# Performance work log

Hardware: AMD Instinct MI355X
Metric: run time of the kernel (lower is better)

The kernel has to match this reference:

```python
import jax, jax.numpy as jnp
import numpy as np

COMMITMENT_COST = 0.25


def setup_inputs() -> dict:
    key = jax.random.key(0)
    k1, k2 = jax.random.split(key)
    B, C, H, W = 64, 64, 32, 32
    K = 1024
    inputs = jax.random.normal(k1, (B, C, H, W), dtype=jnp.float32)
    # matches torch init: uniform_(-1/K, 1/K)
    weight = jax.random.uniform(k2, (K, C), dtype=jnp.float32,
                                minval=-1.0 / K, maxval=1.0 / K)
    return {"inputs": inputs, "weight": weight}


def reference(inputs, weight):
    B, C, H, W = inputs.shape
    # (B H W) C
    flat = inputs.transpose(0, 2, 3, 1).reshape(-1, C)
    distances = (jnp.sum(flat * flat, axis=1, keepdims=True)
                 + jnp.sum(weight * weight, axis=1)
                 - 2.0 * (flat @ weight.T))  # [BHW, K]
    encoding_indices = jnp.argmin(distances, axis=1)  # [BHW]
    # one-hot matmul in the original == direct gather
    quantized = jnp.take(weight, encoding_indices, axis=0)  # [BHW, C]
    quantized = quantized.reshape(B, H, W, C).transpose(0, 3, 1, 2)  # B C H W
    e_latent_loss = jnp.mean(
        (jax.lax.stop_gradient(quantized) - inputs) ** 2, axis=(1, 2, 3))
    q_latent_loss = jnp.mean(
        (quantized - jax.lax.stop_gradient(inputs)) ** 2, axis=(1, 2, 3))
    loss = q_latent_loss + COMMITMENT_COST * e_latent_loss  # [B]
    # straight-through estimator
    quantized_st = inputs + jax.lax.stop_gradient(quantized - inputs)
    indices = encoding_indices.reshape(B, H, W)
    return quantized_st, indices, loss
```

## Files before the change

kernel.cpp:

```cpp
#include <hip/hip_runtime.h>
#include <hip/hip_bf16.h>


#define VQ_C    64
#define VQ_K    1024
#define VQ_HW   1024
#define VQ_B    64
#define VQ_ROWS (VQ_B * VQ_HW)
#define BLOCK   256
#define NBLOCKS (VQ_ROWS / BLOCK)
#define NSEG    4
#define SK      (VQ_K / NSEG)

__global__ __launch_bounds__(BLOCK, 4) void vq_partial_kernel(
    const float* __restrict__ inp,
    const float* __restrict__ w,
    float* __restrict__ dist_ws,
    int*   __restrict__ idx_ws)
{
    __shared__ float se2[SK];

    const int tid = threadIdx.x;
    const int seg = blockIdx.y;
    const int k0  = seg * SK;

    {
        const float* wr = w + (size_t)(k0 + tid) * VQ_C;
        float s0 = 0.f, s1 = 0.f, s2 = 0.f, s3 = 0.f;
        #pragma unroll
        for (int c = 0; c < VQ_C; c += 4) {
            s0 = fmaf(wr[c + 0], wr[c + 0], s0);
            s1 = fmaf(wr[c + 1], wr[c + 1], s1);
            s2 = fmaf(wr[c + 2], wr[c + 2], s2);
            s3 = fmaf(wr[c + 3], wr[c + 3], s3);
        }
        se2[tid] = (s0 + s1) + (s2 + s3);
    }
    __syncthreads();

    const int r  = blockIdx.x * BLOCK + tid;
    const int b  = r >> 10;
    const int hw = r & (VQ_HW - 1);

    const float* xin = inp + (size_t)b * (VQ_C * VQ_HW) + hw;
    float x[VQ_C];
    #pragma unroll
    for (int c = 0; c < VQ_C; ++c) x[c] = xin[(size_t)c * VQ_HW];

    #pragma unroll
    for (int c = 0; c < VQ_C; ++c) asm volatile("" : "+v"(x[c]));

    float sx0 = 0.f, sx1 = 0.f, sx2 = 0.f, sx3 = 0.f;
    #pragma unroll
    for (int c = 0; c < VQ_C; c += 4) {
        sx0 = fmaf(x[c + 0], x[c + 0], sx0);
        sx1 = fmaf(x[c + 1], x[c + 1], sx1);
        sx2 = fmaf(x[c + 2], x[c + 2], sx2);
        sx3 = fmaf(x[c + 3], x[c + 3], sx3);
    }
    const float sx = (sx0 + sx1) + (sx2 + sx3);

    float best  = 3.402823466e38f;
    int   bestk = k0;
    const float* wseg = w + (size_t)k0 * VQ_C;
    #pragma unroll 2
    for (int k = 0; k < SK; ++k) {
        const float* wr = wseg + (size_t)k * VQ_C;
        float d0 = 0.f, d1 = 0.f, d2 = 0.f, d3 = 0.f;
        #pragma unroll
        for (int c = 0; c < VQ_C; c += 4) {
            d0 = fmaf(wr[c + 0], x[c + 0], d0);
            d1 = fmaf(wr[c + 1], x[c + 1], d1);
            d2 = fmaf(wr[c + 2], x[c + 2], d2);
            d3 = fmaf(wr[c + 3], x[c + 3], d3);
        }
        const float dot = (d0 + d1) + (d2 + d3);
        const float d = (sx + se2[k]) - 2.f * dot;
        if (d < best) { best = d; bestk = k0 + k; }
    }

    dist_ws[(size_t)seg * VQ_ROWS + r] = best;
    idx_ws [(size_t)seg * VQ_ROWS + r] = bestk;
}

__global__ __launch_bounds__(BLOCK) void vq_finalize_kernel(
    const float* __restrict__ inp,
    const float* __restrict__ w,
    const float* __restrict__ dist_ws,
    const int*   __restrict__ idx_ws,
    float* __restrict__ out_q,
    float* __restrict__ out_idx,
    float* __restrict__ partials)
{
    __shared__ float red[BLOCK];
    const int tid = threadIdx.x;
    const int r   = blockIdx.x * BLOCK + tid;
    const int b   = r >> 10;
    const int hw  = r & (VQ_HW - 1);

    float best  = dist_ws[r];
    int   bestk = idx_ws[r];
    #pragma unroll
    for (int s = 1; s < NSEG; ++s) {
        const float d  = dist_ws[(size_t)s * VQ_ROWS + r];
        const int   kk = idx_ws [(size_t)s * VQ_ROWS + r];
        if (d < best) { best = d; bestk = kk; }
    }

    const float* xin  = inp + (size_t)b * (VQ_C * VQ_HW) + hw;
    const float* q    = w + (size_t)bestk * VQ_C;
    float*       outr = out_q + (size_t)b * (VQ_C * VQ_HW) + hw;

    float sd0 = 0.f, sd1 = 0.f, sd2 = 0.f, sd3 = 0.f;
    #pragma unroll
    for (int c = 0; c < VQ_C; c += 4) {
        float x0 = xin[(size_t)(c + 0) * VQ_HW];
        float x1 = xin[(size_t)(c + 1) * VQ_HW];
        float x2 = xin[(size_t)(c + 2) * VQ_HW];
        float x3 = xin[(size_t)(c + 3) * VQ_HW];
        float q0 = q[c + 0], q1 = q[c + 1], q2 = q[c + 2], q3 = q[c + 3];
        outr[(size_t)(c + 0) * VQ_HW] = x0 + (q0 - x0);
        outr[(size_t)(c + 1) * VQ_HW] = x1 + (q1 - x1);
        outr[(size_t)(c + 2) * VQ_HW] = x2 + (q2 - x2);
        outr[(size_t)(c + 3) * VQ_HW] = x3 + (q3 - x3);
        float e0 = q0 - x0, e1 = q1 - x1, e2 = q2 - x2, e3 = q3 - x3;
        sd0 = fmaf(e0, e0, sd0);
        sd1 = fmaf(e1, e1, sd1);
        sd2 = fmaf(e2, e2, sd2);
        sd3 = fmaf(e3, e3, sd3);
    }
    out_idx[r] = (float)bestk;

    red[tid] = (sd0 + sd1) + (sd2 + sd3);
    __syncthreads();
    #pragma unroll
    for (int s = BLOCK / 2; s > 0; s >>= 1) {
        if (tid < s) red[tid] += red[tid + s];
        __syncthreads();
    }
    if (tid == 0) partials[blockIdx.x] = red[0];
}

__global__ __launch_bounds__(64) void vq_loss_kernel(
    const float* __restrict__ partials,
    float* __restrict__ loss)
{
    const int b = threadIdx.x;
    const float s = (partials[4 * b + 0] + partials[4 * b + 1])
                  + (partials[4 * b + 2] + partials[4 * b + 3]);
    const float L = s * (1.0f / 65536.0f);
    loss[b] = L + 0.25f * L;
}

__global__ __launch_bounds__(BLOCK) void vq_main_kernel(
    const float* __restrict__ inp,
    const float* __restrict__ w,
    float* __restrict__ out_q,
    float* __restrict__ out_idx,
    float* __restrict__ partials)
{
    __shared__ float se2[VQ_K];
    __shared__ float red[BLOCK];
    const int tid = threadIdx.x;

    for (int k = tid; k < VQ_K; k += BLOCK) {
        const float* wr = w + k * VQ_C;
        float s0 = 0.f, s1 = 0.f, s2 = 0.f, s3 = 0.f;
        #pragma unroll
        for (int c = 0; c < VQ_C; c += 4) {
            s0 = fmaf(wr[c + 0], wr[c + 0], s0);
            s1 = fmaf(wr[c + 1], wr[c + 1], s1);
            s2 = fmaf(wr[c + 2], wr[c + 2], s2);
            s3 = fmaf(wr[c + 3], wr[c + 3], s3);
        }
        se2[k] = (s0 + s1) + (s2 + s3);
    }
    __syncthreads();

    const int r  = blockIdx.x * BLOCK + tid;
    const int b  = r >> 10;
    const int hw = r & (VQ_HW - 1);

    const float* xin = inp + (size_t)b * (VQ_C * VQ_HW) + hw;
    float x[VQ_C];
    #pragma unroll
    for (int c = 0; c < VQ_C; ++c) x[c] = xin[(size_t)c * VQ_HW];
    #pragma unroll
    for (int c = 0; c < VQ_C; ++c) asm volatile("" : "+v"(x[c]));

    float sx0 = 0.f, sx1 = 0.f, sx2 = 0.f, sx3 = 0.f;
    #pragma unroll
    for (int c = 0; c < VQ_C; c += 4) {
        sx0 = fmaf(x[c + 0], x[c + 0], sx0);
        sx1 = fmaf(x[c + 1], x[c + 1], sx1);
        sx2 = fmaf(x[c + 2], x[c + 2], sx2);
        sx3 = fmaf(x[c + 3], x[c + 3], sx3);
    }
    const float sx = (sx0 + sx1) + (sx2 + sx3);

    float best = 3.402823466e38f;
    int bestk = 0;
    for (int k = 0; k < VQ_K; ++k) {
        const float* wr = w + (size_t)k * VQ_C;
        float d0 = 0.f, d1 = 0.f, d2 = 0.f, d3 = 0.f;
        #pragma unroll
        for (int c = 0; c < VQ_C; c += 4) {
            d0 = fmaf(wr[c + 0], x[c + 0], d0);
            d1 = fmaf(wr[c + 1], x[c + 1], d1);
            d2 = fmaf(wr[c + 2], x[c + 2], d2);
            d3 = fmaf(wr[c + 3], x[c + 3], d3);
        }
        const float dot = (d0 + d1) + (d2 + d3);
        const float d = (sx + se2[k]) - 2.f * dot;
        if (d < best) { best = d; bestk = k; }
    }

    const float* q = w + (size_t)bestk * VQ_C;
    float* outr = out_q + (size_t)b * (VQ_C * VQ_HW) + hw;
    float sd0 = 0.f, sd1 = 0.f, sd2 = 0.f, sd3 = 0.f;
    #pragma unroll
    for (int c = 0; c < VQ_C; c += 4) {
        float q0 = q[c + 0], q1 = q[c + 1], q2 = q[c + 2], q3 = q[c + 3];
        float x0 = x[c + 0], x1 = x[c + 1], x2 = x[c + 2], x3 = x[c + 3];
        outr[(size_t)(c + 0) * VQ_HW] = x0 + (q0 - x0);
        outr[(size_t)(c + 1) * VQ_HW] = x1 + (q1 - x1);
        outr[(size_t)(c + 2) * VQ_HW] = x2 + (q2 - x2);
        outr[(size_t)(c + 3) * VQ_HW] = x3 + (q3 - x3);
        float e0 = q0 - x0, e1 = q1 - x1, e2 = q2 - x2, e3 = q3 - x3;
        sd0 = fmaf(e0, e0, sd0);
        sd1 = fmaf(e1, e1, sd1);
        sd2 = fmaf(e2, e2, sd2);
        sd3 = fmaf(e3, e3, sd3);
    }
    out_idx[r] = (float)bestk;

    red[tid] = (sd0 + sd1) + (sd2 + sd3);
    __syncthreads();
    #pragma unroll
    for (int s = BLOCK / 2; s > 0; s >>= 1) {
        if (tid < s) red[tid] += red[tid + s];
        __syncthreads();
    }
    if (tid == 0) partials[blockIdx.x] = red[0];
}

extern "C" void kernel_launch(void* const* d_in, const int* in_sizes, int n_in,
                              void* d_out, int out_size, void* d_ws, size_t ws_size,
                              hipStream_t stream) {
    const float* inp = (const float*)d_in[0];
    const float* w   = (const float*)d_in[1];

    float* out_q    = (float*)d_out;
    float* out_idx  = (float*)d_out + 4194304;
    float* out_loss = (float*)d_out + 4194304 + 65536;

    const size_t dist_bytes = (size_t)NSEG * VQ_ROWS * sizeof(float);
    const size_t idx_bytes  = (size_t)NSEG * VQ_ROWS * sizeof(int);
    const size_t part_bytes = (size_t)NBLOCKS * sizeof(float);
    const size_t need = dist_bytes + idx_bytes + part_bytes;

    if (ws_size >= need) {
        float* dist_ws  = (float*)d_ws;
        int*   idx_ws   = (int*)((char*)d_ws + dist_bytes);
        float* partials = (float*)((char*)d_ws + dist_bytes + idx_bytes);

        vq_partial_kernel<<<dim3(NBLOCKS, NSEG), BLOCK, 0, stream>>>(inp, w, dist_ws, idx_ws);
        vq_finalize_kernel<<<NBLOCKS, BLOCK, 0, stream>>>(inp, w, dist_ws, idx_ws,
                                                          out_q, out_idx, partials);
        vq_loss_kernel<<<1, 64, 0, stream>>>(partials, out_loss);
    } else {
        float* partials = (float*)d_ws;
        vq_main_kernel<<<NBLOCKS, BLOCK, 0, stream>>>(inp, w, out_q, out_idx, partials);
        vq_loss_kernel<<<1, 64, 0, stream>>>(partials, out_loss);
    }
}
```

Baseline: 126.5 us.

## Load codebook rows via scalar s_load into SGPRs and precompute norms in separate kernel

The per-segment codebook norm computation moves into a separate small kernel that writes norms to workspace, removing the shared-memory prologue and barrier from the partial kernel. The inner distance loop now fetches each codebook row (64 floats) and its norm with inline-asm s_load_dwordx16 into scalar registers, so the FMAs take a wave-uniform SGPR operand instead of issuing vector loads. This adds an extra kernel launch and serializes each iteration on an lgkmcnt(0) wait with no unrolling, which may expose scalar-load latency.

```diff
diff --git a/kernel.cpp b/kernel.cpp
--- a/kernel.cpp
+++ b/kernel.cpp
@@ -12,70 +12,94 @@
 #define NSEG    4
 #define SK      (VQ_K / NSEG)
 
-__global__ __launch_bounds__(BLOCK, 4) void vq_partial_kernel(
+typedef float f32x16 __attribute__((ext_vector_type(16)));
+
+#define XC(c) ((c) < 16 ? x0[(c) & 15] : (c) < 32 ? x1[(c) & 15] \
+               : (c) < 48 ? x2[(c) & 15] : x3[(c) & 15])
+#define WC(c) ((c) < 16 ? w0[(c) & 15] : (c) < 32 ? w1[(c) & 15] \
+               : (c) < 48 ? w2[(c) & 15] : w3[(c) & 15])
+
+__global__ __launch_bounds__(BLOCK) void vq_se2_kernel(
+    const float* __restrict__ w, float* __restrict__ se2g) {
+    const int k = blockIdx.x * BLOCK + threadIdx.x;
+    const float* wr = w + (size_t)k * VQ_C;
+    float s0 = 0.f, s1 = 0.f, s2 = 0.f, s3 = 0.f;
+    #pragma unroll
+    for (int c = 0; c < VQ_C; c += 4) {
+        s0 = fmaf(wr[c + 0], wr[c + 0], s0);
+        s1 = fmaf(wr[c + 1], wr[c + 1], s1);
+        s2 = fmaf(wr[c + 2], wr[c + 2], s2);
+        s3 = fmaf(wr[c + 3], wr[c + 3], s3);
+    }
+    se2g[k] = (s0 + s1) + (s2 + s3);
+}
+
+__global__ void
+__attribute__((amdgpu_flat_work_group_size(BLOCK, BLOCK), amdgpu_waves_per_eu(4, 4)))
+vq_partial(
     const float* __restrict__ inp,
     const float* __restrict__ w,
+    const float* __restrict__ se2g,
     float* __restrict__ dist_ws,
     int*   __restrict__ idx_ws)
 {
-    __shared__ float se2[SK];
-
     const int tid = threadIdx.x;
     const int seg = blockIdx.y;
     const int k0  = seg * SK;
 
-    {
-        const float* wr = w + (size_t)(k0 + tid) * VQ_C;
-        float s0 = 0.f, s1 = 0.f, s2 = 0.f, s3 = 0.f;
-        #pragma unroll
-        for (int c = 0; c < VQ_C; c += 4) {
-            s0 = fmaf(wr[c + 0], wr[c + 0], s0);
-            s1 = fmaf(wr[c + 1], wr[c + 1], s1);
-            s2 = fmaf(wr[c + 2], wr[c + 2], s2);
-            s3 = fmaf(wr[c + 3], wr[c + 3], s3);
-        }
-        se2[tid] = (s0 + s1) + (s2 + s3);
-    }
-    __syncthreads();
-
     const int r  = blockIdx.x * BLOCK + tid;
     const int b  = r >> 10;
     const int hw = r & (VQ_HW - 1);
 
     const float* xin = inp + (size_t)b * (VQ_C * VQ_HW) + hw;
-    float x[VQ_C];
-    #pragma unroll
-    for (int c = 0; c < VQ_C; ++c) x[c] = xin[(size_t)c * VQ_HW];
-
-    #pragma unroll
-    for (int c = 0; c < VQ_C; ++c) asm volatile("" : "+v"(x[c]));
+    f32x16 x0, x1, x2, x3;
+    #pragma unroll
+    for (int c = 0; c < 16; ++c) {
+        x0[c] = xin[(size_t)(c +  0) * VQ_HW];
+        x1[c] = xin[(size_t)(c + 16) * VQ_HW];
+        x2[c] = xin[(size_t)(c + 32) * VQ_HW];
+        x3[c] = xin[(size_t)(c + 48) * VQ_HW];
+    }
 
     float sx0 = 0.f, sx1 = 0.f, sx2 = 0.f, sx3 = 0.f;
     #pragma unroll
     for (int c = 0; c < VQ_C; c += 4) {
-        sx0 = fmaf(x[c + 0], x[c + 0], sx0);
-        sx1 = fmaf(x[c + 1], x[c + 1], sx1);
-        sx2 = fmaf(x[c + 2], x[c + 2], sx2);
-        sx3 = fmaf(x[c + 3], x[c + 3], sx3);
+        sx0 = fmaf(XC(c + 0), XC(c + 0), sx0);
+        sx1 = fmaf(XC(c + 1), XC(c + 1), sx1);
+        sx2 = fmaf(XC(c + 2), XC(c + 2), sx2);
+        sx3 = fmaf(XC(c + 3), XC(c + 3), sx3);
     }
     const float sx = (sx0 + sx1) + (sx2 + sx3);
 
     float best  = 3.402823466e38f;
     int   bestk = k0;
-    const float* wseg = w + (size_t)k0 * VQ_C;
-    #pragma unroll 2
-    for (int k = 0; k < SK; ++k) {
-        const float* wr = wseg + (size_t)k * VQ_C;
+    const float* wp = w + (size_t)k0 * VQ_C;
+    const float* sp = se2g + k0;
+
+    #pragma unroll 1
+    for (int k = 0; k < SK; ++k, wp += VQ_C, ++sp) {
+        f32x16 w0, w1, w2, w3;
+        float  se2k;
+        asm volatile(
+            "s_load_dwordx16 %0, %5, 0x0\n\t"
+            "s_load_dwordx16 %1, %5, 0x40\n\t"
+            "s_load_dwordx16 %2, %5, 0x80\n\t"
+            "s_load_dwordx16 %3, %5, 0xc0\n\t"
+            "s_load_dword    %4, %6, 0x0\n\t"
+            "s_waitcnt lgkmcnt(0)"
+            : "=&s"(w0), "=&s"(w1), "=&s"(w2), "=&s"(w3), "=&s"(se2k)
+            : "s"(wp), "s"(sp));
+
         float d0 = 0.f, d1 = 0.f, d2 = 0.f, d3 = 0.f;
         #pragma unroll
         for (int c = 0; c < VQ_C; c += 4) {
-            d0 = fmaf(wr[c + 0], x[c + 0], d0);
-            d1 = fmaf(wr[c + 1], x[c + 1], d1);
-            d2 = fmaf(wr[c + 2], x[c + 2], d2);
-            d3 = fmaf(wr[c + 3], x[c + 3], d3);
+            d0 = fmaf(WC(c + 0), XC(c + 0), d0);
+            d1 = fmaf(WC(c + 1), XC(c + 1), d1);
+            d2 = fmaf(WC(c + 2), XC(c + 2), d2);
+            d3 = fmaf(WC(c + 3), XC(c + 3), d3);
         }
         const float dot = (d0 + d1) + (d2 + d3);
-        const float d = (sx + se2[k]) - 2.f * dot;
+        const float d = (sx + se2k) - 2.f * dot;
         if (d < best) { best = d; bestk = k0 + k; }
     }
 
@@ -90,7 +114,8 @@
     const int*   __restrict__ idx_ws,
     float* __restrict__ out_q,
     float* __restrict__ out_idx,
-    float* __restrict__ partials)
+    float* __restrict__ partials,
+    int nseg)
 {
     __shared__ float red[BLOCK];
     const int tid = threadIdx.x;
@@ -100,8 +125,7 @@
 
     float best  = dist_ws[r];
     int   bestk = idx_ws[r];
-    #pragma unroll
-    for (int s = 1; s < NSEG; ++s) {
+    for (int s = 1; s < nseg; ++s) {
         const float d  = dist_ws[(size_t)s * VQ_ROWS + r];
         const int   kk = idx_ws [(size_t)s * VQ_ROWS + r];
         if (d < best) { best = d; bestk = kk; }
@@ -159,7 +183,7 @@
     float* __restrict__ out_idx,
     float* __restrict__ partials)
 {
-    __shared__ float se2[VQ_K];
+    __shared__ float se2s[VQ_K];
     __shared__ float red[BLOCK];
     const int tid = threadIdx.x;
 
@@ -173,7 +197,7 @@
             s2 = fmaf(wr[c + 2], wr[c + 2], s2);
             s3 = fmaf(wr[c + 3], wr[c + 3], s3);
         }
-        se2[k] = (s0 + s1) + (s2 + s3);
+        se2s[k] = (s0 + s1) + (s2 + s3);
     }
     __syncthreads();
 
@@ -185,8 +209,6 @@
     float x[VQ_C];
     #pragma unroll
     for (int c = 0; c < VQ_C; ++c) x[c] = xin[(size_t)c * VQ_HW];
-    #pragma unroll
-    for (int c = 0; c < VQ_C; ++c) asm volatile("" : "+v"(x[c]));
 
     float sx0 = 0.f, sx1 = 0.f, sx2 = 0.f, sx3 = 0.f;
     #pragma unroll
@@ -211,7 +233,7 @@
             d3 = fmaf(wr[c + 3], x[c + 3], d3);
         }
         const float dot = (d0 + d1) + (d2 + d3);
-        const float d = (sx + se2[k]) - 2.f * dot;
+        const float d = (sx + se2s[k]) - 2.f * dot;
         if (d < best) { best = d; bestk = k; }
     }
 
@@ -254,19 +276,22 @@
     float* out_idx  = (float*)d_out + 4194304;
     float* out_loss = (float*)d_out + 4194304 + 65536;
 
-    const size_t dist_bytes = (size_t)NSEG * VQ_ROWS * sizeof(float);
-    const size_t idx_bytes  = (size_t)NSEG * VQ_ROWS * sizeof(int);
-    const size_t part_bytes = (size_t)NBLOCKS * sizeof(float);
-    const size_t need = dist_bytes + idx_bytes + part_bytes;
+    const size_t se2_f   = VQ_K;
+    const size_t dist_f  = (size_t)NSEG * VQ_ROWS;
+    const size_t idx_f   = (size_t)NSEG * VQ_ROWS;
+    const size_t part_f  = NBLOCKS;
+    const size_t need    = (se2_f + dist_f + idx_f + part_f) * 4;
 
     if (ws_size >= need) {
-        float* dist_ws  = (float*)d_ws;
-        int*   idx_ws   = (int*)((char*)d_ws + dist_bytes);
-        float* partials = (float*)((char*)d_ws + dist_bytes + idx_bytes);
-
-        vq_partial_kernel<<<dim3(NBLOCKS, NSEG), BLOCK, 0, stream>>>(inp, w, dist_ws, idx_ws);
+        float* se2g     = (float*)d_ws;
+        float* dist_ws  = se2g + se2_f;
+        int*   idx_ws   = (int*)(dist_ws + dist_f);
+        float* partials = (float*)(idx_ws + idx_f);
+
+        vq_se2_kernel<<<VQ_K / BLOCK, BLOCK, 0, stream>>>(w, se2g);
+        vq_partial<<<dim3(NBLOCKS, NSEG), BLOCK, 0, stream>>>(inp, w, se2g, dist_ws, idx_ws);
         vq_finalize_kernel<<<NBLOCKS, BLOCK, 0, stream>>>(inp, w, dist_ws, idx_ws,
-                                                          out_q, out_idx, partials);
+                                                          out_q, out_idx, partials, NSEG);
         vq_loss_kernel<<<1, 64, 0, stream>>>(partials, out_loss);
     } else {
         float* partials = (float*)d_ws;
```

Result: no change. 128.0 us (+1.2%).

## Stage codebook segments in LDS and precompute code norms in separate kernel

Applied to the files above, without the earlier changes.

Codebook norms are now computed once by a small kernel instead of in every block. Each partial block copies its codebook segment into shared memory and reads it from there rather than from global/scalar memory. The split can go up to 8 segments when workspace allows, which doubles the partial-result traffic in exchange for more parallelism. The finalize step now breaks ties by lowest index, and the register-pinning asm barriers are removed.

```diff
diff --git a/kernel.cpp b/kernel.cpp
--- a/kernel.cpp
+++ b/kernel.cpp
@@ -9,34 +9,42 @@
 #define VQ_ROWS (VQ_B * VQ_HW)
 #define BLOCK   256
 #define NBLOCKS (VQ_ROWS / BLOCK)
-#define NSEG    4
-#define SK      (VQ_K / NSEG)
-
-__global__ __launch_bounds__(BLOCK, 4) void vq_partial_kernel(
+
+__global__ __launch_bounds__(BLOCK) void vq_se2_kernel(
+    const float* __restrict__ w, float* __restrict__ se2g) {
+    const int k = blockIdx.x * BLOCK + threadIdx.x;
+    const float* wr = w + (size_t)k * VQ_C;
+    float s0 = 0.f, s1 = 0.f, s2 = 0.f, s3 = 0.f;
+    #pragma unroll
+    for (int c = 0; c < VQ_C; c += 4) {
+        s0 = fmaf(wr[c + 0], wr[c + 0], s0);
+        s1 = fmaf(wr[c + 1], wr[c + 1], s1);
+        s2 = fmaf(wr[c + 2], wr[c + 2], s2);
+        s3 = fmaf(wr[c + 3], wr[c + 3], s3);
+    }
+    se2g[k] = (s0 + s1) + (s2 + s3);
+}
+
+template <int SK>
+__global__ __launch_bounds__(BLOCK, 4) void vq_partial_lds(
     const float* __restrict__ inp,
     const float* __restrict__ w,
+    const float* __restrict__ se2g,
     float* __restrict__ dist_ws,
     int*   __restrict__ idx_ws)
 {
-    __shared__ float se2[SK];
+    __shared__ float wl[SK * VQ_C];
+    __shared__ float sl[SK];
 
     const int tid = threadIdx.x;
     const int seg = blockIdx.y;
     const int k0  = seg * SK;
 
-    {
-        const float* wr = w + (size_t)(k0 + tid) * VQ_C;
-        float s0 = 0.f, s1 = 0.f, s2 = 0.f, s3 = 0.f;
-        #pragma unroll
-        for (int c = 0; c < VQ_C; c += 4) {
-            s0 = fmaf(wr[c + 0], wr[c + 0], s0);
-            s1 = fmaf(wr[c + 1], wr[c + 1], s1);
-            s2 = fmaf(wr[c + 2], wr[c + 2], s2);
-            s3 = fmaf(wr[c + 3], wr[c + 3], s3);
-        }
-        se2[tid] = (s0 + s1) + (s2 + s3);
-    }
-    __syncthreads();
+    const float* wsegp = w + (size_t)k0 * VQ_C;
+    #pragma unroll
+    for (int i = 0; i < (SK * VQ_C) / BLOCK; ++i)
+        wl[i * BLOCK + tid] = wsegp[i * BLOCK + tid];
+    if (tid < SK) sl[tid] = se2g[k0 + tid];
 
     const int r  = blockIdx.x * BLOCK + tid;
     const int b  = r >> 10;
@@ -46,9 +54,6 @@
     float x[VQ_C];
     #pragma unroll
     for (int c = 0; c < VQ_C; ++c) x[c] = xin[(size_t)c * VQ_HW];
-
-    #pragma unroll
-    for (int c = 0; c < VQ_C; ++c) asm volatile("" : "+v"(x[c]));
 
     float sx0 = 0.f, sx1 = 0.f, sx2 = 0.f, sx3 = 0.f;
     #pragma unroll
@@ -60,12 +65,13 @@
     }
     const float sx = (sx0 + sx1) + (sx2 + sx3);
 
+    __syncthreads();
+
     float best  = 3.402823466e38f;
     int   bestk = k0;
-    const float* wseg = w + (size_t)k0 * VQ_C;
-    #pragma unroll 2
+    #pragma unroll 1
     for (int k = 0; k < SK; ++k) {
-        const float* wr = wseg + (size_t)k * VQ_C;
+        const float* wr = &wl[k * VQ_C];
         float d0 = 0.f, d1 = 0.f, d2 = 0.f, d3 = 0.f;
         #pragma unroll
         for (int c = 0; c < VQ_C; c += 4) {
@@ -75,7 +81,7 @@
             d3 = fmaf(wr[c + 3], x[c + 3], d3);
         }
         const float dot = (d0 + d1) + (d2 + d3);
-        const float d = (sx + se2[k]) - 2.f * dot;
+        const float d = (sx + sl[k]) - 2.f * dot;
         if (d < best) { best = d; bestk = k0 + k; }
     }
 
@@ -90,7 +96,8 @@
     const int*   __restrict__ idx_ws,
     float* __restrict__ out_q,
     float* __restrict__ out_idx,
-    float* __restrict__ partials)
+    float* __restrict__ partials,
+    int nseg)
 {
     __shared__ float red[BLOCK];
     const int tid = threadIdx.x;
@@ -100,11 +107,10 @@
 
     float best  = dist_ws[r];
     int   bestk = idx_ws[r];
-    #pragma unroll
-    for (int s = 1; s < NSEG; ++s) {
+    for (int s = 1; s < nseg; ++s) {
         const float d  = dist_ws[(size_t)s * VQ_ROWS + r];
         const int   kk = idx_ws [(size_t)s * VQ_ROWS + r];
-        if (d < best) { best = d; bestk = kk; }
+        if (d < best || (d == best && kk < bestk)) { best = d; bestk = kk; }
     }
 
     const float* xin  = inp + (size_t)b * (VQ_C * VQ_HW) + hw;
@@ -159,7 +165,7 @@
     float* __restrict__ out_idx,
     float* __restrict__ partials)
 {
-    __shared__ float se2[VQ_K];
+    __shared__ float se2s[VQ_K];
     __shared__ float red[BLOCK];
     const int tid = threadIdx.x;
 
@@ -173,7 +179,7 @@
             s2 = fmaf(wr[c + 2], wr[c + 2], s2);
             s3 = fmaf(wr[c + 3], wr[c + 3], s3);
         }
-        se2[k] = (s0 + s1) + (s2 + s3);
+        se2s[k] = (s0 + s1) + (s2 + s3);
     }
     __syncthreads();
 
@@ -185,8 +191,6 @@
     float x[VQ_C];
     #pragma unroll
     for (int c = 0; c < VQ_C; ++c) x[c] = xin[(size_t)c * VQ_HW];
-    #pragma unroll
-    for (int c = 0; c < VQ_C; ++c) asm volatile("" : "+v"(x[c]));
 
     float sx0 = 0.f, sx1 = 0.f, sx2 = 0.f, sx3 = 0.f;
     #pragma unroll
@@ -211,7 +215,7 @@
             d3 = fmaf(wr[c + 3], x[c + 3], d3);
         }
         const float dot = (d0 + d1) + (d2 + d3);
-        const float d = (sx + se2[k]) - 2.f * dot;
+        const float d = (sx + se2s[k]) - 2.f * dot;
         if (d < best) { best = d; bestk = k; }
     }
 
@@ -254,19 +258,32 @@
     float* out_idx  = (float*)d_out + 4194304;
     float* out_loss = (float*)d_out + 4194304 + 65536;
 
-    const size_t dist_bytes = (size_t)NSEG * VQ_ROWS * sizeof(float);
-    const size_t idx_bytes  = (size_t)NSEG * VQ_ROWS * sizeof(int);
-    const size_t part_bytes = (size_t)NBLOCKS * sizeof(float);
-    const size_t need = dist_bytes + idx_bytes + part_bytes;
-
-    if (ws_size >= need) {
-        float* dist_ws  = (float*)d_ws;
-        int*   idx_ws   = (int*)((char*)d_ws + dist_bytes);
-        float* partials = (float*)((char*)d_ws + dist_bytes + idx_bytes);
-
-        vq_partial_kernel<<<dim3(NBLOCKS, NSEG), BLOCK, 0, stream>>>(inp, w, dist_ws, idx_ws);
+    const size_t se2_f  = VQ_K;
+    const size_t part_f = NBLOCKS;
+    auto need = [&](int ns) {
+        return (se2_f + (size_t)ns * VQ_ROWS * 2 + part_f) * 4;
+    };
+
+    int nseg = 0;
+    if (ws_size >= need(8))      nseg = 8;
+    else if (ws_size >= need(4)) nseg = 4;
+
+    if (nseg > 0) {
+        float* se2g     = (float*)d_ws;
+        float* dist_ws  = se2g + se2_f;
+        int*   idx_ws   = (int*)(dist_ws + (size_t)nseg * VQ_ROWS);
+        float* partials = (float*)((int*)idx_ws + (size_t)nseg * VQ_ROWS);
+
+        vq_se2_kernel<<<VQ_K / BLOCK, BLOCK, 0, stream>>>(w, se2g);
+        if (nseg == 8) {
+            vq_partial_lds<VQ_K / 8><<<dim3(NBLOCKS, 8), BLOCK, 0, stream>>>(
+                inp, w, se2g, dist_ws, idx_ws);
+        } else {
+            vq_partial_lds<VQ_K / 4><<<dim3(NBLOCKS, 4), BLOCK, 0, stream>>>(
+                inp, w, se2g, dist_ws, idx_ws);
+        }
         vq_finalize_kernel<<<NBLOCKS, BLOCK, 0, stream>>>(inp, w, dist_ws, idx_ws,
-                                                          out_q, out_idx, partials);
+                                                          out_q, out_idx, partials, nseg);
         vq_loss_kernel<<<1, 64, 0, stream>>>(partials, out_loss);
     } else {
         float* partials = (float*)d_ws;
```

After: 159.8 us. +26.3%, slower.
